# Kernel optimization log

Measured on AMD Instinct MI355X. Metric: run time of the kernel, lower is better.

## Reference

```python
import jax, jax.numpy as jnp
import numpy as np

B, DX, DY, H, K = 16384, 128, 128, 2048, 16
MIN_BIN = 1e-3   # min bin width/height (nflows convention)
MIN_DERIV = 1e-3  # min knot derivative


def setup_inputs() -> dict:
    key = jax.random.key(0)
    k0, k1, k2, k3 = jax.random.split(key, 4)
    x = jax.random.normal(k0, (B, DX), jnp.float32)
    y = jax.random.uniform(k1, (B, DY), jnp.float32, minval=1e-4, maxval=1.0 - 1e-4)
    W1 = jax.random.normal(k2, (DX, H), jnp.float32) / np.sqrt(DX).astype(np.float32)
    b1 = jnp.zeros((H,), jnp.float32)
    W2 = jax.random.normal(k3, (H, DY * (3 * K + 1)), jnp.float32) / np.sqrt(H).astype(np.float32)
    b2 = jnp.zeros((DY * (3 * K + 1),), jnp.float32)
    return {"x": x, "y": y, "W1": W1, "b1": b1, "W2": W2, "b2": b2}


def _rq_spline(y, pdf):
    # y: [B, D] in (0,1); pdf: [B, D, 3K+1] unnormalized spline params
    w_un, h_un, d_un = pdf[..., :K], pdf[..., K:2 * K], pdf[..., 2 * K:]
    widths = MIN_BIN + (1.0 - K * MIN_BIN) * jax.nn.softmax(w_un, axis=-1)   # [B,D,K]
    heights = MIN_BIN + (1.0 - K * MIN_BIN) * jax.nn.softmax(h_un, axis=-1)  # [B,D,K]
    derivs = MIN_DERIV + jax.nn.softplus(d_un)                               # [B,D,K+1]

    pad = [(0, 0), (0, 0), (1, 0)]
    cw = jnp.pad(jnp.cumsum(widths, axis=-1), pad)    # knot x-positions [B,D,K+1]
    ch = jnp.pad(jnp.cumsum(heights, axis=-1), pad)   # knot y-positions [B,D,K+1]

    # data-dependent bin lookup (searchsorted equivalent, vectorized)
    idx = jnp.clip(jnp.sum(y[..., None] >= cw, axis=-1) - 1, 0, K - 1)  # [B,D]
    g = lambda a: jnp.take_along_axis(a, idx[..., None], axis=-1)[..., 0]
    xk, yk = g(cw), g(ch)
    wk, hk = g(widths), g(heights)
    dk = g(derivs)
    dk1 = jnp.take_along_axis(derivs, idx[..., None] + 1, axis=-1)[..., 0]

    s = hk / wk                      # bin slope
    t = (y - xk) / wk                # theta in [0,1]
    omt = 1.0 - t
    denom = s + (dk1 + dk - 2.0 * s) * t * omt
    out = yk + hk * (s * t * t + dk * t * omt) / denom
    deriv = s * s * (dk1 * t * t + 2.0 * s * t * omt + dk * omt * omt) / (denom * denom)
    dlogp = jnp.sum(jnp.log(deriv), axis=-1, keepdims=True)  # [B,1]
    return out, dlogp


def reference(x, y, W1, b1, W2, b2):
    # conditioner MLP: x -> spline params
    h = jax.nn.relu(x @ W1 + b1)
    pdf = (h @ W2 + b2).reshape(x.shape[0], DY, 3 * K + 1)
    return _rq_spline(y, pdf)
```

## Files before the change

### kernel.cpp

```cpp
#include <hip/hip_runtime.h>
#include <hip/hip_fp16.h>
#include <cstdint>
#include <cstddef>

#define B_ROWS 16384
#define DX 128
#define DYDIM 128
#define HDIM 2048
#define NPARAM 49
#define NCOL 6272
#define NTILES 26
#define W2PROWS (NTILES * 256)

typedef __attribute__((ext_vector_type(8))) _Float16 half8v;
typedef __attribute__((ext_vector_type(4))) float f32x4;

__global__ void k_f32_to_f16(const float* __restrict__ in, _Float16* __restrict__ out, int n) {
  int i = blockIdx.x * 256 + threadIdx.x;
  if (i < n) out[i] = (_Float16)in[i];
}

__global__ void k_transpose_f16(const float* __restrict__ in, _Float16* __restrict__ out, int R, int C) {
  __shared__ float tile[32][33];
  int c0 = blockIdx.x * 32, r0 = blockIdx.y * 32;
  int tx = threadIdx.x;
  for (int i = threadIdx.y; i < 32; i += 8)
    tile[i][tx] = in[(size_t)(r0 + i) * C + c0 + tx];
  __syncthreads();
  for (int i = threadIdx.y; i < 32; i += 8)
    out[(size_t)(c0 + i) * R + r0 + tx] = (_Float16)tile[tx][i];
}

__global__ void k_transpose_perm(const float* __restrict__ in, _Float16* __restrict__ out) {
  __shared__ float tile[32][33];
  int c0 = blockIdx.x * 32, r0 = blockIdx.y * 32;
  int tx = threadIdx.x;
  for (int i = threadIdx.y; i < 32; i += 8)
    tile[i][tx] = in[(size_t)(r0 + i) * NCOL + c0 + tx];
  __syncthreads();
  for (int i = threadIdx.y; i < 32; i += 8) {
    int g = c0 + i;
    int t = g / 245;
    int cc = g - t * 245;
    out[(size_t)(t * 256 + cc) * HDIM + r0 + tx] = (_Float16)tile[tx][i];
  }
}

__global__ __launch_bounds__(256) void k_gemm1(
    const _Float16* __restrict__ A, const _Float16* __restrict__ Bt,
    const float* __restrict__ bias, _Float16* __restrict__ C,
    int M, int N, int K) {
  __shared__ _Float16 Abuf[128 * 32];
  __shared__ _Float16 Bbuf[128 * 32];
  const int t = threadIdx.x;
  const int l = t & 63;
  const int w = t >> 6;
  int bx = blockIdx.x, by = blockIdx.y;
  {
    const int nx = gridDim.x;
    const int nwg = nx * gridDim.y;
    const int lin = by * nx + bx;
    const int cpx = nwg >> 3;
    const int sw = (lin & 7) * cpx + (lin >> 3);
    bx = sw % nx;
    by = sw / nx;
  }
  const int tileM = by * 128;
  const int tileN = bx * 128;
  const int wm = w >> 1, wn = w & 1;
  const int srow = w * 16 + (l >> 2);
  const int skel = (l & 3) * 8;
  const char* Ag = (const char*)(A + (size_t)(tileM + srow) * K + skel);
  const char* Bg = (const char*)(Bt + (size_t)(tileN + srow) * K + skel);
  const size_t gRowStep = (size_t)64 * K * 2;
  auto ldsA = (__attribute__((address_space(3))) char*)Abuf;
  auto ldsB = (__attribute__((address_space(3))) char*)Bbuf;
  const int ldsBase = w * 1024;
  f32x4 acc[4][4];
#pragma unroll
  for (int i = 0; i < 4; ++i)
#pragma unroll
    for (int j = 0; j < 4; ++j) acc[i][j] = (f32x4){0.f, 0.f, 0.f, 0.f};
  const int nk = K >> 5;
#define STAGE1(kt)                                                                             \
  do {                                                                                         \
    size_t koff = (size_t)(kt) * 64;                                                           \
    __builtin_amdgcn_global_load_lds(                                                          \
        (const __attribute__((address_space(1))) uint32_t*)(Ag + koff),                        \
        (__attribute__((address_space(3))) uint32_t*)(ldsA + ldsBase), 16, 0, 0);              \
    __builtin_amdgcn_global_load_lds(                                                          \
        (const __attribute__((address_space(1))) uint32_t*)(Ag + koff + gRowStep),             \
        (__attribute__((address_space(3))) uint32_t*)(ldsA + 4096 + ldsBase), 16, 0, 0);       \
    __builtin_amdgcn_global_load_lds(                                                          \
        (const __attribute__((address_space(1))) uint32_t*)(Bg + koff),                        \
        (__attribute__((address_space(3))) uint32_t*)(ldsB + ldsBase), 16, 0, 0);              \
    __builtin_amdgcn_global_load_lds(                                                          \
        (const __attribute__((address_space(1))) uint32_t*)(Bg + koff + gRowStep),             \
        (__attribute__((address_space(3))) uint32_t*)(ldsB + 4096 + ldsBase), 16, 0, 0);       \
  } while (0)
  STAGE1(0);
  const int abase = (wm * 64 + (l & 15)) * 32 + (l >> 4) * 8;
  const int bbase = (wn * 64 + (l & 15)) * 32 + (l >> 4) * 8;
  for (int kt = 0; kt < nk; ++kt) {
    __syncthreads();
    half8v av[4], bv[4];
#pragma unroll
    for (int mf = 0; mf < 4; ++mf)
      av[mf] = *(const half8v*)((const _Float16*)Abuf + abase + mf * 512);
#pragma unroll
    for (int nf = 0; nf < 4; ++nf)
      bv[nf] = *(const half8v*)((const _Float16*)Bbuf + bbase + nf * 512);
#pragma unroll
    for (int mf = 0; mf < 4; ++mf)
#pragma unroll
      for (int nf = 0; nf < 4; ++nf)
        acc[mf][nf] = __builtin_amdgcn_mfma_f32_16x16x32_f16(av[mf], bv[nf], acc[mf][nf], 0, 0, 0);
    __syncthreads();
    if (kt + 1 < nk) STAGE1(kt + 1);
  }
#undef STAGE1
  const int crow0 = tileM + wm * 64 + (l >> 4) * 4;
  const int ccol0 = tileN + wn * 64 + (l & 15);
#pragma unroll
  for (int nf = 0; nf < 4; ++nf) {
    const int col = ccol0 + nf * 16;
    const float bvv = bias[col];
#pragma unroll
    for (int mf = 0; mf < 4; ++mf) {
#pragma unroll
      for (int j = 0; j < 4; ++j) {
        const int row = crow0 + mf * 16 + j;
        float v = fmaxf(acc[mf][nf][j] + bvv, 0.f);
        C[(size_t)row * N + col] = (_Float16)v;
      }
    }
  }
}

__global__ __launch_bounds__(512, 2) void k_gemm2s(
    const _Float16* __restrict__ A, const _Float16* __restrict__ Bt,
    const float* __restrict__ bias, const float* __restrict__ y,
    float* __restrict__ outp, float* __restrict__ gpart, int M) {
  constexpr int K = HDIM;
  constexpr int K2 = K * 2;
  constexpr int NT = K / 64;
  constexpr int ITERS = NT / 2;

  __shared__ char smem[131072];
  __shared__ float red[512];

  const int t = threadIdx.x;
  const int l = t & 63;
  const int w = t >> 6;
  const int wm = w >> 2;
  const int wn = w & 3;
  const int rlo = l & 15;
  const int khi = l >> 4;
  const int wOff = w * 1024;

  int bx = blockIdx.x, by = blockIdx.y;
  {
    const int lin = by * 26 + bx;
    const int xcd = lin & 7;
    const int slot = lin >> 3;
    bx = slot >> 3;
    by = xcd * 8 + (slot & 7);
  }
  const int tileM = by * 256;
  const int tileN = bx * 256;

  int rowj[2], kbj[2];
#pragma unroll
  for (int j = 0; j < 2; ++j) {
    const int phys = j * 8192 + t * 16;
    const int b = phys ^ (((phys >> 9) & 1) << 5);
    rowj[j] = ((b >> 11) << 4) + ((b >> 6) & 15);
    kbj[j] = (((b >> 10) & 1) << 6) + (b & 63);
  }
  const char* pA[2][2];
  const char* pB[2][2];
#pragma unroll
  for (int half = 0; half < 2; ++half)
#pragma unroll
    for (int j = 0; j < 2; ++j) {
      pA[half][j] = (const char*)A + (size_t)(tileM + half * 128 + rowj[j]) * K2 + kbj[j];
      pB[half][j] = (const char*)Bt + (size_t)(tileN + half * 128 + rowj[j]) * K2 + kbj[j];
    }

  auto lds3 = (__attribute__((address_space(3))) char*)smem;

#define LDSA(d, half) ((d) * 32768 + (half) * 16384)
#define LDSB(d, half) (65536 + (d) * 32768 + (half) * 16384)
#define GLDS(srcp, ldsoff)                                                                   \
  __builtin_amdgcn_global_load_lds(                                                           \
      (const __attribute__((address_space(1))) uint32_t*)(srcp),                              \
      (__attribute__((address_space(3))) uint32_t*)(lds3 + (ldsoff) + wOff), 16, 0, 0)
#define STG(op, d, half, kt)                                                                  \
  do {                                                                                        \
    GLDS(p##op[half][0] + (size_t)(kt) * 128, LDS##op(d, half));                              \
    GLDS(p##op[half][1] + (size_t)(kt) * 128, LDS##op(d, half) + 8192);                       \
  } while (0)
#define VM(n) asm volatile("s_waitcnt vmcnt(" #n ")" ::: "memory")
#define NOSTG ((void)0)
#define NOW ((void)0)
#define NORD ((void)0)
#define CFENCE asm volatile("" ::: "memory")

  const int swz = (rlo & 8) ? 32 : 0;
  const int lane16 = rlo * 64 + ((khi * 16) ^ swz);
  const int aW = wm * 8192 + lane16;
  const int bW = 65536 + wn * 4096 + lane16;

  half8v b000, b001, b010, b011, b100, b101, b110, b111;
  half8v s0_0, s0_1, s0_2, s0_3;
  half8v s1_0, s1_1, s1_2, s1_3;

  f32x4 acc[8][4];
#pragma unroll
  for (int i = 0; i < 8; ++i)
#pragma unroll
    for (int j = 0; j < 4; ++j) acc[i][j] = (f32x4){0.f, 0.f, 0.f, 0.f};

#define MF(fi, gj, av, bv) \
  acc[fi][gj] = __builtin_amdgcn_mfma_f32_16x16x32_f16(av, bv, acc[fi][gj], 0, 0, 0)

#define RDA(S, d, q)                                                                          \
  do {                                                                                        \
    const int aB = (d) * 32768 + ((q) >> 1) * 16384 + ((q) & 1) * 4096 + aW;                  \
    S##_0 = *(const half8v*)(smem + aB);                                                      \
    S##_1 = *(const half8v*)(smem + aB + 1024);                                               \
    S##_2 = *(const half8v*)(smem + aB + 2048);                                               \
    S##_3 = *(const half8v*)(smem + aB + 3072);                                               \
  } while (0)

#define HDRB(d)                                                                               \
  do {                                                                                        \
    const int bB = (d) * 32768 + bW;                                                          \
    b000 = *(const half8v*)(smem + bB);                                                       \
    b001 = *(const half8v*)(smem + bB + 1024);                                                \
    b010 = *(const half8v*)(smem + bB + 2048);                                                \
    b011 = *(const half8v*)(smem + bB + 3072);                                                \
    b100 = *(const half8v*)(smem + bB + 16384);                                               \
    b101 = *(const half8v*)(smem + bB + 17408);                                               \
    b110 = *(const half8v*)(smem + bB + 18432);                                               \
    b111 = *(const half8v*)(smem + bB + 19456);                                               \
  } while (0)

#define MFQ(q, S)                                                                             \
  {                                                                                           \
    constexpr int f0 = ((q) >> 1) * 4 + ((q) & 1) * 2;                                        \
    MF(f0 + 0, 0, S##_0, b000); MF(f0 + 0, 1, S##_0, b010);                                   \
    MF(f0 + 0, 2, S##_0, b100); MF(f0 + 0, 3, S##_0, b110);                                   \
    MF(f0 + 1, 0, S##_2, b000); MF(f0 + 1, 1, S##_2, b010);                                   \
    MF(f0 + 1, 2, S##_2, b100); MF(f0 + 1, 3, S##_2, b110);                                   \
    MF(f0 + 0, 0, S##_1, b001); MF(f0 + 0, 1, S##_1, b011);                                   \
    MF(f0 + 0, 2, S##_1, b101); MF(f0 + 0, 3, S##_1, b111);                                   \
    MF(f0 + 1, 0, S##_3, b001); MF(f0 + 1, 1, S##_3, b011);                                   \
    MF(f0 + 1, 2, S##_3, b101); MF(f0 + 1, 3, S##_3, b111);                                   \
  }

#define PH2(STAGES, WAITS, RD, MFMAS)                                                         \
  do {                                                                                        \
    STAGES;                                                                                   \
    WAITS;                                                                                    \
    CFENCE;                                                                                   \
    __builtin_amdgcn_s_barrier();                                                             \
    CFENCE;                                                                                   \
    RD;                                                                                       \
    __builtin_amdgcn_s_setprio(1);                                                            \
    MFMAS;                                                                                    \
    __builtin_amdgcn_s_setprio(0);                                                            \
    CFENCE;                                                                                   \
    __builtin_amdgcn_s_barrier();                                                             \
  } while (0)

  STG(B, 0, 0, 0);
  STG(B, 0, 1, 0);
  STG(A, 0, 0, 0);
  STG(A, 0, 1, 0);
  STG(B, 1, 0, 1);
  STG(B, 1, 1, 1);
  STG(A, 1, 0, 1);
  VM(6);
  CFENCE;
  __builtin_amdgcn_s_barrier();
  RDA(s0, 0, 0);

  for (int it = 0; it < ITERS - 1; ++it) {
    const int kt = 2 * it;
    PH2(HDRB(0); STG(A, 1, 1, kt + 1), NOW, RDA(s1, 0, 1), MFQ(0, s0));
    PH2(STG(B, 0, 0, kt + 2), NOW, RDA(s0, 0, 2), MFQ(1, s1));
    PH2(STG(B, 0, 1, kt + 2); STG(A, 0, 0, kt + 2), NOW, RDA(s1, 0, 3), MFQ(2, s0));
    PH2(NOSTG, VM(8), RDA(s0, 1, 0), MFQ(3, s1));
    PH2(HDRB(1); STG(A, 0, 1, kt + 2), NOW, RDA(s1, 1, 1), MFQ(0, s0));
    PH2(STG(B, 1, 0, kt + 3), VM(10), RDA(s0, 1, 2), MFQ(1, s1));
    PH2(STG(B, 1, 1, kt + 3); STG(A, 1, 0, kt + 3), NOW, RDA(s1, 1, 3), MFQ(2, s0));
    PH2(NOSTG, VM(6), RDA(s0, 0, 0), MFQ(3, s1));
  }
  PH2(HDRB(0); STG(A, 1, 1, NT - 1), NOW, RDA(s1, 0, 1), MFQ(0, s0));
  PH2(NOSTG, NOW, RDA(s0, 0, 2), MFQ(1, s1));
  PH2(NOSTG, NOW, RDA(s1, 0, 3), MFQ(2, s0));
  PH2(NOSTG, VM(2), RDA(s0, 1, 0), MFQ(3, s1));
  PH2(HDRB(1), NOW, RDA(s1, 1, 1), MFQ(0, s0));
  PH2(NOSTG, VM(0), RDA(s0, 1, 2), MFQ(1, s1));
  PH2(NOSTG, NOW, RDA(s1, 1, 3), MFQ(2, s0));
  PH2(NOSTG, NOW, NORD, MFQ(3, s1));

#undef PH2
#undef MFQ
#undef HDRB
#undef RDA
#undef MF
#undef STG
#undef GLDS
#undef LDSA
#undef LDSB

  const int RCt = (bx < 25) ? 245 : 147;
  const int nd  = (bx < 25) ? 5 : 3;

#pragma unroll
  for (int fi = 0; fi < 8; ++fi) {
    const int r0l = (((fi >> 2) * 2 + wm) << 6) + ((fi & 3) << 4) + khi * 4;
#pragma unroll
    for (int gj = 0; gj < 4; ++gj) {
      const int c = (((gj >> 1) * 4 + wn) << 5) + ((gj & 1) << 4) + rlo;
      if (c < RCt) {
        const float bvv = bias[245 * bx + c];
        const int cb = c * 512;
        const int cs = (c & 31) << 4;
#pragma unroll
        for (int jp = 0; jp < 2; ++jp) {
          const int r = r0l + jp * 2;
          const unsigned short lo =
              __builtin_bit_cast(unsigned short, (_Float16)(acc[fi][gj][jp * 2] + bvv));
          const unsigned short hi =
              __builtin_bit_cast(unsigned short, (_Float16)(acc[fi][gj][jp * 2 + 1] + bvv));
          *(uint32_t*)(smem + cb + ((2 * r) ^ cs)) = (uint32_t)lo | ((uint32_t)hi << 16);
        }
      }
    }
  }
  __syncthreads();

  const int r = t & 255;
  const int rg = tileM + r;
  float yv_[3];
#pragma unroll
  for (int pass = 0; pass < 3; ++pass) {
    const int d = pass * 2 + (t >> 8);
    yv_[pass] = (d < nd) ? y[(size_t)rg * DYDIM + 5 * bx + d] : 0.f;
  }

#define LDC(p) ((float)*(const _Float16*)(smem + (size_t)(dD * 49 + (p)) * 512 + \
                                          ((2 * r) ^ (((dD * 49 + (p)) & 31) << 4))))
  float lsum = 0.f;
#pragma unroll
  for (int pass = 0; pass < 3; ++pass) {
    const int dD = pass * 2 + (t >> 8);
    if (dD < nd) {
      float qw[16], qh[16], qd[17];
#pragma unroll
      for (int p = 0; p < 16; ++p) { qw[p] = LDC(p); qh[p] = LDC(16 + p); }
#pragma unroll
      for (int p = 0; p < 17; ++p) qd[p] = LDC(32 + p);

      float mw = qw[0], mh = qh[0];
#pragma unroll
      for (int p = 1; p < 16; ++p) { mw = fmaxf(mw, qw[p]); mh = fmaxf(mh, qh[p]); }
      float ew[16], eh[16];
      float sw2 = 0.f, sh = 0.f;
#pragma unroll
      for (int p = 0; p < 16; ++p) {
        ew[p] = __expf(qw[p] - mw);
        eh[p] = __expf(qh[p] - mh);
        sw2 += ew[p];
        sh += eh[p];
      }
      const float rw = 0.984f / sw2, rh = 0.984f / sh;
      const float yv = yv_[pass];

      float cws = 0.f, chs = 0.f, xk = 0.f, yk = 0.f, wk = 1.f, hk = 1.f;
      float du0 = qd[0], du1 = qd[1];
#pragma unroll
      for (int j = 0; j < 16; ++j) {
        float wj = 0.001f + rw * ew[j];
        float hj = 0.001f + rh * eh[j];
        if (yv >= cws) { xk = cws; yk = chs; wk = wj; hk = hj; du0 = qd[j]; du1 = qd[j + 1]; }
        cws += wj;
        chs += hj;
      }
      const float dk  = 0.001f + fmaxf(du0, 0.f) + log1pf(__expf(-fabsf(du0)));
      const float dk1 = 0.001f + fmaxf(du1, 0.f) + log1pf(__expf(-fabsf(du1)));

      const float s = hk / wk;
      const float tt = (yv - xk) / wk;
      const float omt = 1.f - tt;
      const float dnm = s + (dk1 + dk - 2.f * s) * tt * omt;
      const float o = yk + hk * (s * tt * tt + dk * tt * omt) / dnm;
      const float dr = s * s * (dk1 * tt * tt + 2.f * s * tt * omt + dk * omt * omt) / (dnm * dnm);

      outp[(size_t)rg * DYDIM + 5 * bx + dD] = o;
      lsum += __logf(dr);
    }
  }
#undef LDC
  red[t] = lsum;
  __syncthreads();
  if (t < 256)
    gpart[(size_t)bx * B_ROWS + (tileM + t)] = red[t] + red[t + 256];
}

__global__ void k_dlogp_reduce(const float* __restrict__ gpart, float* __restrict__ dlogp) {
  int b = blockIdx.x * 256 + threadIdx.x;
  float s = 0.f;
  for (int tt = 0; tt < NTILES; ++tt) s += gpart[(size_t)tt * B_ROWS + b];
  dlogp[b] = s;
}

extern "C" void kernel_launch(void* const* d_in, const int* in_sizes, int n_in,
                              void* d_out, int out_size, void* d_ws, size_t ws_size,
                              hipStream_t stream) {
  const float* x  = (const float*)d_in[0];
  const float* y  = (const float*)d_in[1];
  const float* W1 = (const float*)d_in[2];
  const float* b1 = (const float*)d_in[3];
  const float* W2 = (const float*)d_in[4];
  const float* b2 = (const float*)d_in[5];
  float* out = (float*)d_out;
  float* dlogp = out + (size_t)B_ROWS * DYDIM;

  char* ws = (char*)d_ws;
  _Float16* w2p = (_Float16*)ws;
  _Float16* h   = w2p + (size_t)W2PROWS * HDIM;
  _Float16* xb  = h + (size_t)B_ROWS * HDIM;
  _Float16* w1t = xb + (size_t)B_ROWS * DX;
  float* gpart  = (float*)(w1t + (size_t)HDIM * DX);

  k_f32_to_f16<<<(B_ROWS * DX + 255) / 256, 256, 0, stream>>>(x, xb, B_ROWS * DX);
  k_transpose_f16<<<dim3(HDIM / 32, DX / 32), dim3(32, 8), 0, stream>>>(W1, w1t, DX, HDIM);
  k_transpose_perm<<<dim3(NCOL / 32, HDIM / 32), dim3(32, 8), 0, stream>>>(W2, w2p);

  k_gemm1<<<dim3(HDIM / 128, B_ROWS / 128), 256, 0, stream>>>(
      xb, w1t, b1, h, B_ROWS, HDIM, DX);

  k_gemm2s<<<dim3(NTILES, B_ROWS / 256), 512, 0, stream>>>(
      h, w2p, b2, y, out, gpart, B_ROWS);

  k_dlogp_reduce<<<B_ROWS / 256, 256, 0, stream>>>(gpart, dlogp);
}
```

Measured before the change: 547.4 us.

## Merge GEMM phases into two-quarter regions to halve barrier count

Restructures the main GEMM loop so each barrier-delimited region covers two A quarters instead of one. This halves the number of s_barrier pairs per K step. The first A quarter is read before the barrier and the second is read between the two MFMA groups. The global-to-LDS staging is regrouped and the vmcnt waits are adjusted to match. The risk is less overlap of LDS reads with MFMAs, plus possible hazards if the changed wait and stage placement does not match buffer reuse.

```diff
diff --git a/kernel.cpp b/kernel.cpp
--- a/kernel.cpp
+++ b/kernel.cpp
@@ -203,7 +203,6 @@
 #define VM(n) asm volatile("s_waitcnt vmcnt(" #n ")" ::: "memory")
 #define NOSTG ((void)0)
 #define NOW ((void)0)
-#define NORD ((void)0)
 #define CFENCE asm volatile("" ::: "memory")
 
   const int swz = (rlo & 8) ? 32 : 0;
@@ -212,9 +211,6 @@
   const int bW = 65536 + wn * 4096 + lane16;
 
   half8v b000, b001, b010, b011, b100, b101, b110, b111;
-  half8v s0_0, s0_1, s0_2, s0_3;
-  half8v s1_0, s1_1, s1_2, s1_3;
-
   f32x4 acc[8][4];
 #pragma unroll
   for (int i = 0; i < 8; ++i)
@@ -224,13 +220,13 @@
 #define MF(fi, gj, av, bv) \
   acc[fi][gj] = __builtin_amdgcn_mfma_f32_16x16x32_f16(av, bv, acc[fi][gj], 0, 0, 0)
 
-#define RDA(S, d, q)                                                                          \
+#define RD4(v0, v1, v2, v3, d, q)                                                             \
   do {                                                                                        \
     const int aB = (d) * 32768 + ((q) >> 1) * 16384 + ((q) & 1) * 4096 + aW;                  \
-    S##_0 = *(const half8v*)(smem + aB);                                                      \
-    S##_1 = *(const half8v*)(smem + aB + 1024);                                               \
-    S##_2 = *(const half8v*)(smem + aB + 2048);                                               \
-    S##_3 = *(const half8v*)(smem + aB + 3072);                                               \
+    v0 = *(const half8v*)(smem + aB);                                                         \
+    v1 = *(const half8v*)(smem + aB + 1024);                                                  \
+    v2 = *(const half8v*)(smem + aB + 2048);                                                  \
+    v3 = *(const half8v*)(smem + aB + 3072);                                                  \
   } while (0)
 
 #define HDRB(d)                                                                               \
@@ -246,29 +242,35 @@
     b111 = *(const half8v*)(smem + bB + 19456);                                               \
   } while (0)
 
-#define MFQ(q, S)                                                                             \
+#define MFQ4(q, v0, v1, v2, v3)                                                               \
   {                                                                                           \
     constexpr int f0 = ((q) >> 1) * 4 + ((q) & 1) * 2;                                        \
-    MF(f0 + 0, 0, S##_0, b000); MF(f0 + 0, 1, S##_0, b010);                                   \
-    MF(f0 + 0, 2, S##_0, b100); MF(f0 + 0, 3, S##_0, b110);                                   \
-    MF(f0 + 1, 0, S##_2, b000); MF(f0 + 1, 1, S##_2, b010);                                   \
-    MF(f0 + 1, 2, S##_2, b100); MF(f0 + 1, 3, S##_2, b110);                                   \
-    MF(f0 + 0, 0, S##_1, b001); MF(f0 + 0, 1, S##_1, b011);                                   \
-    MF(f0 + 0, 2, S##_1, b101); MF(f0 + 0, 3, S##_1, b111);                                   \
-    MF(f0 + 1, 0, S##_3, b001); MF(f0 + 1, 1, S##_3, b011);                                   \
-    MF(f0 + 1, 2, S##_3, b101); MF(f0 + 1, 3, S##_3, b111);                                   \
-  }
-
-#define PH2(STAGES, WAITS, RD, MFMAS)                                                         \
+    MF(f0 + 0, 0, v0, b000); MF(f0 + 0, 1, v0, b010);                                         \
+    MF(f0 + 0, 2, v0, b100); MF(f0 + 0, 3, v0, b110);                                         \
+    MF(f0 + 1, 0, v2, b000); MF(f0 + 1, 1, v2, b010);                                         \
+    MF(f0 + 1, 2, v2, b100); MF(f0 + 1, 3, v2, b110);                                         \
+    MF(f0 + 0, 0, v1, b001); MF(f0 + 0, 1, v1, b011);                                         \
+    MF(f0 + 0, 2, v1, b101); MF(f0 + 0, 3, v1, b111);                                         \
+    MF(f0 + 1, 0, v3, b001); MF(f0 + 1, 1, v3, b011);                                         \
+    MF(f0 + 1, 2, v3, b101); MF(f0 + 1, 3, v3, b111);                                         \
+  }
+
+#define REGION(d, HDR, qa, qb, STAGES, WAITS)                                                 \
   do {                                                                                        \
+    half8v x0, x1, x2, x3, z0, z1, z2, z3;                                                    \
+    RD4(x0, x1, x2, x3, d, qa);                                                               \
+    if (HDR) HDRB(d);                                                                         \
     STAGES;                                                                                   \
     WAITS;                                                                                    \
     CFENCE;                                                                                   \
     __builtin_amdgcn_s_barrier();                                                             \
     CFENCE;                                                                                   \
-    RD;                                                                                       \
     __builtin_amdgcn_s_setprio(1);                                                            \
-    MFMAS;                                                                                    \
+    MFQ4(qa, x0, x1, x2, x3);                                                                 \
+    __builtin_amdgcn_s_setprio(0);                                                            \
+    RD4(z0, z1, z2, z3, d, qb);                                                               \
+    __builtin_amdgcn_s_setprio(1);                                                            \
+    MFQ4(qb, z0, z1, z2, z3);                                                                 \
     __builtin_amdgcn_s_setprio(0);                                                            \
     CFENCE;                                                                                   \
     __builtin_amdgcn_s_barrier();                                                             \
@@ -284,32 +286,23 @@
   VM(6);
   CFENCE;
   __builtin_amdgcn_s_barrier();
-  RDA(s0, 0, 0);
 
   for (int it = 0; it < ITERS - 1; ++it) {
     const int kt = 2 * it;
-    PH2(HDRB(0); STG(A, 1, 1, kt + 1), NOW, RDA(s1, 0, 1), MFQ(0, s0));
-    PH2(STG(B, 0, 0, kt + 2), NOW, RDA(s0, 0, 2), MFQ(1, s1));
-    PH2(STG(B, 0, 1, kt + 2); STG(A, 0, 0, kt + 2), NOW, RDA(s1, 0, 3), MFQ(2, s0));
-    PH2(NOSTG, VM(8), RDA(s0, 1, 0), MFQ(3, s1));
-    PH2(HDRB(1); STG(A, 0, 1, kt + 2), NOW, RDA(s1, 1, 1), MFQ(0, s0));
-    PH2(STG(B, 1, 0, kt + 3), VM(10), RDA(s0, 1, 2), MFQ(1, s1));
-    PH2(STG(B, 1, 1, kt + 3); STG(A, 1, 0, kt + 3), NOW, RDA(s1, 1, 3), MFQ(2, s0));
-    PH2(NOSTG, VM(6), RDA(s0, 0, 0), MFQ(3, s1));
-  }
-  PH2(HDRB(0); STG(A, 1, 1, NT - 1), NOW, RDA(s1, 0, 1), MFQ(0, s0));
-  PH2(NOSTG, NOW, RDA(s0, 0, 2), MFQ(1, s1));
-  PH2(NOSTG, NOW, RDA(s1, 0, 3), MFQ(2, s0));
-  PH2(NOSTG, VM(2), RDA(s0, 1, 0), MFQ(3, s1));
-  PH2(HDRB(1), NOW, RDA(s1, 1, 1), MFQ(0, s0));
-  PH2(NOSTG, VM(0), RDA(s0, 1, 2), MFQ(1, s1));
-  PH2(NOSTG, NOW, RDA(s1, 1, 3), MFQ(2, s0));
-  PH2(NOSTG, NOW, NORD, MFQ(3, s1));
-
-#undef PH2
-#undef MFQ
+    REGION(0, 1, 0, 1, STG(A, 1, 1, kt + 1); STG(B, 0, 0, kt + 2), NOW);
+    REGION(0, 0, 2, 3, STG(B, 0, 1, kt + 2); STG(A, 0, 0, kt + 2), VM(8));
+    REGION(1, 1, 0, 1, STG(A, 0, 1, kt + 2); STG(B, 1, 0, kt + 3), VM(10));
+    REGION(1, 0, 2, 3, STG(B, 1, 1, kt + 3); STG(A, 1, 0, kt + 3), VM(6));
+  }
+  REGION(0, 1, 0, 1, STG(A, 1, 1, NT - 1), NOW);
+  REGION(0, 0, 2, 3, NOSTG, VM(2));
+  REGION(1, 1, 0, 1, NOSTG, VM(0));
+  REGION(1, 0, 2, 3, NOSTG, NOW);
+
+#undef REGION
+#undef MFQ4
 #undef HDRB
-#undef RDA
+#undef RD4
 #undef MF
 #undef STG
 #undef GLDS
```

Result: faster. 488.3 us, median of 2 (-10.8%).
